# Performance work log

Hardware: AMD Instinct MI355X
Metric: run time of the kernel (lower is better)

Reference implementation:

```python
import jax, jax.numpy as jnp
import numpy as np

TABLE_SIZE = 256
I16_MIN, I16_MAX = -32768.0, 32767.0
I8_MIN, I8_MAX = -128.0, 127.0
MAX_SOFTMAX_VALUE = 1.0
OUT_SCALE = MAX_SOFTMAX_VALUE * 2.0 / 255.0            # int8 output scale
EXP_OUT_SCALE = 2.0 / 65535.0                          # qint16 exp output scale
RECIP_OUT_SCALE = (1.0 / 0.1) * 2.0 / 65535.0          # qint16 reciprocal output scale
# (xmin, xmax, kind) in ascending x order; 'table' = 256-entry LUT, 'line' = linear fit
EXP_REGIONS = [(-40.0, -20.0, 'line'), (-20.0, -10.0, 'table'), (-10.0, 0.0, 'table'), (0.0, 1.0, 'line')]
RECIP_REGIONS = [(0.001, 0.1, 'line'), (0.1, 250.0, 'table'), (250.0, 500.0, 'table'), (500.0, 700.0, 'line')]


def _quant(y, out_scale, qmin, qmax):
    return jnp.clip(jnp.round(y / out_scale), qmin, qmax)


def _piecewise(x, func, regions, out_scale, qmin, qmax):
    """Piecewise quantized approximation of func: constant / line / 256-entry
    table regions, returning quantized (integer-valued float) outputs."""
    left_c = _quant(func(jnp.float32(regions[0][0])), out_scale, qmin, qmax)
    y = left_c * jnp.ones_like(x)
    for xmin, xmax, kind in regions:
        if kind == 'table':
            xs = jnp.linspace(xmin, xmax, TABLE_SIZE)
            tab = _quant(func(xs), out_scale, qmin, qmax)
            idx = jnp.clip(jnp.round((x - xmin) * ((TABLE_SIZE - 1) / (xmax - xmin))), 0, TABLE_SIZE - 1).astype(jnp.int32)
            y_r = tab[idx]
        else:
            y0 = func(jnp.float32(xmin))
            y1 = func(jnp.float32(xmax))
            y_r = _quant(y0 + (x - xmin) * ((y1 - y0) / (xmax - xmin)), out_scale, qmin, qmax)
        y = jnp.where(x >= xmin, y_r, y)
    right_c = _quant(func(jnp.float32(regions[-1][1])), out_scale, qmin, qmax)
    return jnp.where(x > regions[-1][1], right_c, y)


def setup_inputs() -> dict:
    key = jax.random.key(0)
    k1, _ = jax.random.split(key)
    data = jax.random.randint(k1, (32, 128, 80, 80), -128, 128, dtype=jnp.int32)  # int8 repr, zp=0
    data_scale = jnp.array([0.0625], dtype=jnp.float32)
    return {"data": data, "data_scale": data_scale}


def reference(data, data_scale):
    ds = data_scale[0]
    C = data.shape[1]
    shift = float(np.ceil(np.log2(C)))  # rescale_shift for the exp-sum
    # max-subtract in the integer domain, dequantize diff (zero_point = 0)
    qmax = jnp.max(data, axis=1, keepdims=True)
    xd = (data - qmax).astype(jnp.float32) * ds  # [B,C,H,W], in (-inf, 0]
    # quantized exp via piecewise tables -> qint16 with EXP_OUT_SCALE
    exp_q = _piecewise(xd, jnp.exp, EXP_REGIONS, EXP_OUT_SCALE, I16_MIN, I16_MAX)
    # sum over channels, right-shift back into int16 range
    sum_q = jnp.sum(exp_q, axis=1, keepdims=True)
    sum_sh = jnp.clip(jnp.round(sum_q * (2.0 ** -shift)), I16_MIN, I16_MAX)
    div_scale = EXP_OUT_SCALE * (2.0 ** shift)  # div_data_scale
    # quantized reciprocal of the (dequantized) shifted sum -> qint16
    recip_q = _piecewise(sum_sh * div_scale, lambda v: 1.0 / v, RECIP_REGIONS, RECIP_OUT_SCALE, I16_MIN, I16_MAX)
    # out = exp * recip, requantized to int8 with OUT_SCALE, then dequantized
    out_q = jnp.clip(jnp.round(exp_q * recip_q * (EXP_OUT_SCALE * RECIP_OUT_SCALE / OUT_SCALE)), I8_MIN, I8_MAX)
    return out_q * OUT_SCALE
```

## Files before the change

kernel.cpp:

```cpp
#include <hip/hip_runtime.h>
#include <cmath>

#define NB  32
#define NC  128
#define NHW 6400
#define PIX 64
#define TPB 256

typedef float vfloat4 __attribute__((ext_vector_type(4)));


__global__ __launch_bounds__(TPB) void qsoftmax_kernel(
    const int* __restrict__ data,
    const float* __restrict__ dscale,
    float* __restrict__ out) {
#pragma clang fp contract(off)
  __shared__ int   exp_tab[256];
  __shared__ float recip_tab[256];
  __shared__ int4  red_m[16][16];
  __shared__ int4  red_s[16][16];

  const int t  = threadIdx.x;
  const int k  = t >> 4;
  const int p4 = t & 15;

  const int blk  = blockIdx.x;
  const int b    = blk / (NHW / PIX);
  const int hw0  = (blk % (NHW / PIX)) * PIX;
  const int base4 = b * NC * (NHW / 4) + (hw0 >> 2);

  const float ds = dscale[0];

  {
    const float EXP_SCALE_F = (float)(2.0 / 65535.0);
    float x = (float)(-t) * ds;
    float e;
    if (x >= 0.0f) {
      float y0 = expf(0.0f), y1 = expf(1.0f);
      e = rintf((y0 + x * ((y1 - y0) / 1.0f)) / EXP_SCALE_F);
    } else if (x >= -10.0f) {
      float delta = 10.0f / 255.0f;
      float idxf = rintf((x + 10.0f) * 25.5f);
      idxf = fminf(fmaxf(idxf, 0.0f), 255.0f);
      float xs = -10.0f + idxf * delta;
      e = rintf((float)exp((double)xs) / EXP_SCALE_F);
    } else {
      float delta = 10.0f / 255.0f;
      float idxf = rintf((x + 20.0f) * 25.5f);
      idxf = fminf(fmaxf(idxf, 0.0f), 255.0f);
      float xs = -20.0f + idxf * delta;
      e = rintf((float)exp((double)xs) / EXP_SCALE_F);
    }
    e = fminf(fmaxf(e, -32768.0f), 32767.0f);
    exp_tab[t] = (int)e;

    const float RECIP_SCALE_F = (float)((1.0 / 0.1) * 2.0 / 65535.0);
    float deltar = (250.0f - 0.1f) / 255.0f;
    float xs = 0.1f + (float)t * deltar;
    float r = rintf((1.0f / xs) / RECIP_SCALE_F);
    r = fminf(fmaxf(r, -32768.0f), 32767.0f);
    recip_tab[t] = r;
  }

  const int4* g4 = (const int4*)data;
  int pd[8];
  int4 m = make_int4(-128, -128, -128, -128);
#pragma unroll
  for (int i = 0; i < 8; ++i) {
    int4 v = g4[base4 + (16 * i + k) * (NHW / 4) + p4];
    m.x = max(m.x, v.x); m.y = max(m.y, v.y);
    m.z = max(m.z, v.z); m.w = max(m.w, v.w);
    pd[i] = (v.x & 255) | ((v.y & 255) << 8) | ((v.z & 255) << 16) |
            (int)((unsigned)(v.w & 255) << 24);
  }
  red_m[k][p4] = m;
  __syncthreads();

  int4 q = red_m[0][p4];
#pragma unroll
  for (int kk = 1; kk < 16; ++kk) {
    int4 r = red_m[kk][p4];
    q.x = max(q.x, r.x); q.y = max(q.y, r.y);
    q.z = max(q.z, r.z); q.w = max(q.w, r.w);
  }

  int pe[16];
  int4 s = make_int4(0, 0, 0, 0);
#pragma unroll
  for (int i = 0; i < 8; ++i) {
    int pdv = pd[i];
    int c0 = (pdv << 24) >> 24;
    int c1 = (pdv << 16) >> 24;
    int c2 = (pdv << 8) >> 24;
    int c3 = pdv >> 24;
    int e0 = exp_tab[q.x - c0];
    int e1 = exp_tab[q.y - c1];
    int e2 = exp_tab[q.z - c2];
    int e3 = exp_tab[q.w - c3];
    s.x += e0; s.y += e1; s.z += e2; s.w += e3;
    pe[2 * i]     = e0 | (e1 << 16);
    pe[2 * i + 1] = e2 | (e3 << 16);
  }
  red_s[k][p4] = s;
  __syncthreads();

  int4 tot = red_s[0][p4];
#pragma unroll
  for (int kk = 1; kk < 16; ++kk) {
    int4 r = red_s[kk][p4];
    tot.x += r.x; tot.y += r.y; tot.z += r.z; tot.w += r.w;
  }
  const float DIV_SCALE_F = (float)((2.0 / 65535.0) * 128.0);
  const float RIDX_K_F    = (float)(255.0 / (250.0 - 0.1));
  float rq[4];
  {
    int tv[4] = {tot.x, tot.y, tot.z, tot.w};
#pragma unroll
    for (int j = 0; j < 4; ++j) {
      float ss = rintf((float)tv[j] * 0.0078125f);
      ss = fminf(fmaxf(ss, -32768.0f), 32767.0f);
      float v = ss * DIV_SCALE_F;
      float idxf = rintf((v - 0.1f) * RIDX_K_F);
      idxf = fminf(fmaxf(idxf, 0.0f), 255.0f);
      rq[j] = recip_tab[(int)idxf];
    }
  }

  const float K_F = (float)((2.0 / 65535.0) * ((1.0 / 0.1) * 2.0 / 65535.0) / (2.0 / 255.0));
  const float OUT_SCALE_F = (float)(2.0 / 255.0);
  vfloat4* o4 = (vfloat4*)out;
#pragma unroll
  for (int i = 0; i < 8; ++i) {
    int pa = pe[2 * i], pb = pe[2 * i + 1];
    float e0 = (float)(pa & 0xFFFF);
    float e1 = (float)(pa >> 16);
    float e2 = (float)(pb & 0xFFFF);
    float e3 = (float)(pb >> 16);
    vfloat4 o;
    o.x = fminf(fmaxf(rintf((e0 * rq[0]) * K_F), -128.0f), 127.0f) * OUT_SCALE_F;
    o.y = fminf(fmaxf(rintf((e1 * rq[1]) * K_F), -128.0f), 127.0f) * OUT_SCALE_F;
    o.z = fminf(fmaxf(rintf((e2 * rq[2]) * K_F), -128.0f), 127.0f) * OUT_SCALE_F;
    o.w = fminf(fmaxf(rintf((e3 * rq[3]) * K_F), -128.0f), 127.0f) * OUT_SCALE_F;
    __builtin_nontemporal_store(o, &o4[base4 + (16 * i + k) * (NHW / 4) + p4]);
  }
}

extern "C" void kernel_launch(void* const* d_in, const int* in_sizes, int n_in,
                              void* d_out, int out_size, void* d_ws, size_t ws_size,
                              hipStream_t stream) {
  const int* data     = (const int*)d_in[0];
  const float* dscale = (const float*)d_in[1];
  float* out          = (float*)d_out;
  (void)in_sizes; (void)n_in; (void)d_ws; (void)ws_size; (void)out_size;

  dim3 grid(NB * (NHW / PIX));
  qsoftmax_kernel<<<grid, TPB, 0, stream>>>(data, dscale, out);
}
```

Baseline: 187.8 us.

## Process two pixel tiles per block with software-pipelined loads and SWAR index math

Each block now handles two 64-pixel tiles. The second tile's loads are issued right after the first max reduction, so they overlap the first tile's exp and sum work, and the block count is halved. Table indices are now computed with packed-byte SWAR subtraction instead of per-channel sign extension. The cost is higher register pressure from holding a second tile of int4 values, which may reduce occupancy, and roughly half as many blocks.

```diff
diff --git a/kernel.cpp b/kernel.cpp
--- a/kernel.cpp
+++ b/kernel.cpp
@@ -1,11 +1,12 @@
 #include <hip/hip_runtime.h>
 #include <cmath>
 
-#define NB  32
-#define NC  128
-#define NHW 6400
-#define PIX 64
-#define TPB 256
+#define NB    32
+#define NC    128
+#define NHW   6400
+#define PIX   64
+#define TPB   256
+#define PAIRS 50
 
 typedef float vfloat4 __attribute__((ext_vector_type(4)));
 
@@ -23,12 +24,6 @@
   const int t  = threadIdx.x;
   const int k  = t >> 4;
   const int p4 = t & 15;
-
-  const int blk  = blockIdx.x;
-  const int b    = blk / (NHW / PIX);
-  const int hw0  = (blk % (NHW / PIX)) * PIX;
-  const int base4 = b * NC * (NHW / 4) + (hw0 >> 2);
-
   const float ds = dscale[0];
 
   {
@@ -62,19 +57,36 @@
     recip_tab[t] = r;
   }
 
-  const int4* g4 = (const int4*)data;
-  int pd[8];
-  int4 m = make_int4(-128, -128, -128, -128);
-#pragma unroll
-  for (int i = 0; i < 8; ++i) {
-    int4 v = g4[base4 + (16 * i + k) * (NHW / 4) + p4];
-    m.x = max(m.x, v.x); m.y = max(m.y, v.y);
-    m.z = max(m.z, v.z); m.w = max(m.w, v.w);
-    pd[i] = (v.x & 255) | ((v.y & 255) << 8) | ((v.z & 255) << 16) |
-            (int)((unsigned)(v.w & 255) << 24);
-  }
-  red_m[k][p4] = m;
-  __syncthreads();
+  const int blk   = blockIdx.x;
+  const int b     = blk / PAIRS;
+  const int pair  = blk % PAIRS;
+  const int base4 = b * NC * (NHW / 4) + pair * 32 + p4;
+  const int4* g4  = (const int4*)data;
+  vfloat4* o4     = (vfloat4*)out;
+
+  const float DIV_SCALE_F = (float)((2.0 / 65535.0) * 128.0);
+  const float RIDX_K_F    = (float)(255.0 / (250.0 - 0.1));
+  const float K_F = (float)((2.0 / 65535.0) * ((1.0 / 0.1) * 2.0 / 65535.0) / (2.0 / 255.0));
+  const float OUT_SCALE_F = (float)(2.0 / 255.0);
+
+  int pd0[8];
+  int4 m0 = make_int4(-128, -128, -128, -128);
+#pragma unroll
+  for (int i = 0; i < 8; ++i) {
+    int4 v = g4[base4 + (16 * i + k) * (NHW / 4)];
+    m0.x = max(m0.x, v.x); m0.y = max(m0.y, v.y);
+    m0.z = max(m0.z, v.z); m0.w = max(m0.w, v.w);
+    pd0[i] = (v.x & 255) | ((v.y & 255) << 8) | ((v.z & 255) << 16) |
+             (int)((unsigned)(v.w & 255) << 24);
+  }
+  red_m[k][p4] = m0;
+  __syncthreads();
+
+  int4 v1[8];
+#pragma unroll
+  for (int i = 0; i < 8; ++i) {
+    v1[i] = g4[base4 + 16 + (16 * i + k) * (NHW / 4)];
+  }
 
   int4 q = red_m[0][p4];
 #pragma unroll
@@ -84,24 +96,32 @@
     q.z = max(q.z, r.z); q.w = max(q.w, r.w);
   }
 
-  int pe[16];
-  int4 s = make_int4(0, 0, 0, 0);
-#pragma unroll
-  for (int i = 0; i < 8; ++i) {
-    int pdv = pd[i];
-    int c0 = (pdv << 24) >> 24;
-    int c1 = (pdv << 16) >> 24;
-    int c2 = (pdv << 8) >> 24;
-    int c3 = pdv >> 24;
-    int e0 = exp_tab[q.x - c0];
-    int e1 = exp_tab[q.y - c1];
-    int e2 = exp_tab[q.z - c2];
-    int e3 = exp_tab[q.w - c3];
-    s.x += e0; s.y += e1; s.z += e2; s.w += e3;
-    pe[2 * i]     = e0 | (e1 << 16);
-    pe[2 * i + 1] = e2 | (e3 << 16);
-  }
-  red_s[k][p4] = s;
+  {
+    unsigned Qe = (((unsigned)q.x & 255u) | (((unsigned)q.z & 255u) << 16)) + 0x01000100u;
+    unsigned Qo = ((((unsigned)q.y & 255u) << 8) | (((unsigned)q.w & 255u) << 24)) + 0x00010000u;
+#pragma unroll
+    for (int i = 0; i < 8; ++i) {
+      unsigned pp = (unsigned)pd0[i];
+      unsigned je = (Qe - (pp & 0x00FF00FFu)) & 0x00FF00FFu;
+      unsigned jo = (Qo - (pp & 0xFF00FF00u)) & 0xFF00FF00u;
+      pd0[i] = (int)(je | jo);
+    }
+  }
+
+  int pe0[16];
+  int4 s0 = make_int4(0, 0, 0, 0);
+#pragma unroll
+  for (int i = 0; i < 8; ++i) {
+    unsigned J = (unsigned)pd0[i];
+    int e0 = exp_tab[J & 255u];
+    int e1 = exp_tab[(J >> 8) & 255u];
+    int e2 = exp_tab[(J >> 16) & 255u];
+    int e3 = exp_tab[J >> 24];
+    s0.x += e0; s0.y += e1; s0.z += e2; s0.w += e3;
+    pe0[2 * i]     = e0 | (e1 << 16);
+    pe0[2 * i + 1] = e2 | (e3 << 16);
+  }
+  red_s[k][p4] = s0;
   __syncthreads();
 
   int4 tot = red_s[0][p4];
@@ -110,9 +130,7 @@
     int4 r = red_s[kk][p4];
     tot.x += r.x; tot.y += r.y; tot.z += r.z; tot.w += r.w;
   }
-  const float DIV_SCALE_F = (float)((2.0 / 65535.0) * 128.0);
-  const float RIDX_K_F    = (float)(255.0 / (250.0 - 0.1));
-  float rq[4];
+  float rq0[4];
   {
     int tv[4] = {tot.x, tot.y, tot.z, tot.w};
 #pragma unroll
@@ -122,26 +140,106 @@
       float v = ss * DIV_SCALE_F;
       float idxf = rintf((v - 0.1f) * RIDX_K_F);
       idxf = fminf(fmaxf(idxf, 0.0f), 255.0f);
-      rq[j] = recip_tab[(int)idxf];
-    }
-  }
-
-  const float K_F = (float)((2.0 / 65535.0) * ((1.0 / 0.1) * 2.0 / 65535.0) / (2.0 / 255.0));
-  const float OUT_SCALE_F = (float)(2.0 / 255.0);
-  vfloat4* o4 = (vfloat4*)out;
-#pragma unroll
-  for (int i = 0; i < 8; ++i) {
-    int pa = pe[2 * i], pb = pe[2 * i + 1];
+      rq0[j] = recip_tab[(int)idxf];
+    }
+  }
+
+  int pd1[8];
+  int4 m1 = make_int4(-128, -128, -128, -128);
+#pragma unroll
+  for (int i = 0; i < 8; ++i) {
+    int4 v = v1[i];
+    m1.x = max(m1.x, v.x); m1.y = max(m1.y, v.y);
+    m1.z = max(m1.z, v.z); m1.w = max(m1.w, v.w);
+    pd1[i] = (v.x & 255) | ((v.y & 255) << 8) | ((v.z & 255) << 16) |
+             (int)((unsigned)(v.w & 255) << 24);
+  }
+  red_m[k][p4] = m1;
+  __syncthreads();
+
+#pragma unroll
+  for (int i = 0; i < 8; ++i) {
+    int pa = pe0[2 * i], pb = pe0[2 * i + 1];
     float e0 = (float)(pa & 0xFFFF);
     float e1 = (float)(pa >> 16);
     float e2 = (float)(pb & 0xFFFF);
     float e3 = (float)(pb >> 16);
     vfloat4 o;
-    o.x = fminf(fmaxf(rintf((e0 * rq[0]) * K_F), -128.0f), 127.0f) * OUT_SCALE_F;
-    o.y = fminf(fmaxf(rintf((e1 * rq[1]) * K_F), -128.0f), 127.0f) * OUT_SCALE_F;
-    o.z = fminf(fmaxf(rintf((e2 * rq[2]) * K_F), -128.0f), 127.0f) * OUT_SCALE_F;
-    o.w = fminf(fmaxf(rintf((e3 * rq[3]) * K_F), -128.0f), 127.0f) * OUT_SCALE_F;
-    __builtin_nontemporal_store(o, &o4[base4 + (16 * i + k) * (NHW / 4) + p4]);
+    o.x = fminf(fmaxf(rintf((e0 * rq0[0]) * K_F), -128.0f), 127.0f) * OUT_SCALE_F;
+    o.y = fminf(fmaxf(rintf((e1 * rq0[1]) * K_F), -128.0f), 127.0f) * OUT_SCALE_F;
+    o.z = fminf(fmaxf(rintf((e2 * rq0[2]) * K_F), -128.0f), 127.0f) * OUT_SCALE_F;
+    o.w = fminf(fmaxf(rintf((e3 * rq0[3]) * K_F), -128.0f), 127.0f) * OUT_SCALE_F;
+    __builtin_nontemporal_store(o, &o4[base4 + (16 * i + k) * (NHW / 4)]);
+  }
+
+  int4 q1 = red_m[0][p4];
+#pragma unroll
+  for (int kk = 1; kk < 16; ++kk) {
+    int4 r = red_m[kk][p4];
+    q1.x = max(q1.x, r.x); q1.y = max(q1.y, r.y);
+    q1.z = max(q1.z, r.z); q1.w = max(q1.w, r.w);
+  }
+  {
+    unsigned Qe = (((unsigned)q1.x & 255u) | (((unsigned)q1.z & 255u) << 16)) + 0x01000100u;
+    unsigned Qo = ((((unsigned)q1.y & 255u) << 8) | (((unsigned)q1.w & 255u) << 24)) + 0x00010000u;
+#pragma unroll
+    for (int i = 0; i < 8; ++i) {
+      unsigned pp = (unsigned)pd1[i];
+      unsigned je = (Qe - (pp & 0x00FF00FFu)) & 0x00FF00FFu;
+      unsigned jo = (Qo - (pp & 0xFF00FF00u)) & 0xFF00FF00u;
+      pd1[i] = (int)(je | jo);
+    }
+  }
+
+  int pe1[16];
+  int4 s1 = make_int4(0, 0, 0, 0);
+#pragma unroll
+  for (int i = 0; i < 8; ++i) {
+    unsigned J = (unsigned)pd1[i];
+    int e0 = exp_tab[J & 255u];
+    int e1 = exp_tab[(J >> 8) & 255u];
+    int e2 = exp_tab[(J >> 16) & 255u];
+    int e3 = exp_tab[J >> 24];
+    s1.x += e0; s1.y += e1; s1.z += e2; s1.w += e3;
+    pe1[2 * i]     = e0 | (e1 << 16);
+    pe1[2 * i + 1] = e2 | (e3 << 16);
+  }
+  red_s[k][p4] = s1;
+  __syncthreads();
+
+  int4 tot1 = red_s[0][p4];
+#pragma unroll
+  for (int kk = 1; kk < 16; ++kk) {
+    int4 r = red_s[kk][p4];
+    tot1.x += r.x; tot1.y += r.y; tot1.z += r.z; tot1.w += r.w;
+  }
+  float rq1[4];
+  {
+    int tv[4] = {tot1.x, tot1.y, tot1.z, tot1.w};
+#pragma unroll
+    for (int j = 0; j < 4; ++j) {
+      float ss = rintf((float)tv[j] * 0.0078125f);
+      ss = fminf(fmaxf(ss, -32768.0f), 32767.0f);
+      float v = ss * DIV_SCALE_F;
+      float idxf = rintf((v - 0.1f) * RIDX_K_F);
+      idxf = fminf(fmaxf(idxf, 0.0f), 255.0f);
+      rq1[j] = recip_tab[(int)idxf];
+    }
+  }
+
+#pragma unroll
+  for (int i = 0; i < 8; ++i) {
+    int pa = pe1[2 * i], pb = pe1[2 * i + 1];
+    float e0 = (float)(pa & 0xFFFF);
+    float e1 = (float)(pa >> 16);
+    float e2 = (float)(pb & 0xFFFF);
+    float e3 = (float)(pb >> 16);
+    vfloat4 o;
+    o.x = fminf(fmaxf(rintf((e0 * rq1[0]) * K_F), -128.0f), 127.0f) * OUT_SCALE_F;
+    o.y = fminf(fmaxf(rintf((e1 * rq1[1]) * K_F), -128.0f), 127.0f) * OUT_SCALE_F;
+    o.z = fminf(fmaxf(rintf((e2 * rq1[2]) * K_F), -128.0f), 127.0f) * OUT_SCALE_F;
+    o.w = fminf(fmaxf(rintf((e3 * rq1[3]) * K_F), -128.0f), 127.0f) * OUT_SCALE_F;
+    __builtin_nontemporal_store(o, &o4[base4 + 16 + (16 * i + k) * (NHW / 4)]);
   }
 }
 
@@ -153,6 +251,6 @@
   float* out          = (float*)d_out;
   (void)in_sizes; (void)n_in; (void)d_ws; (void)ws_size; (void)out_size;
 
-  dim3 grid(NB * (NHW / PIX));
+  dim3 grid(NB * PAIRS);
   qsoftmax_kernel<<<grid, TPB, 0, stream>>>(data, dscale, out);
 }
```

Measured after the change: 188.8 us. No clear change (+0.6%).
